# Performance work log

Hardware: AMD Instinct MI355X
Metric: run time of the kernel (lower is better)

## Reference

```python
import jax, jax.numpy as jnp
import numpy as np

# Dims: L list entries, T hutch samples, D = output_dim*inducing_size, H = 16 hidden
L, T, D, H = 32, 64, 8192, 16


def setup_inputs() -> dict:
    key = jax.random.key(0)
    k = jax.random.split(key, 4)
    return {
        "u": jax.random.normal(k[0], (L, D), jnp.float32),
        "w": jax.random.normal(k[1], (L, T, D), jnp.float32),  # Hutchinson Gaussian probes
        "W1": jax.random.normal(k[2], (H, D), jnp.float32) / np.sqrt(D).astype(np.float32),
        "b1": jnp.zeros((H,), jnp.float32),
        "W2": jax.random.normal(k[3], (D, H), jnp.float32) / np.sqrt(H).astype(np.float32),
        "b2": jnp.zeros((D,), jnp.float32),
    }


def reference(u, w, W1, b1, W2, b2):
    # f = W2 tanh(W1 u + b1) + b2 ; Jacobian J = W2 diag(1 - h^2) W1
    h = jnp.tanh(u @ W1.T + b1)                 # [L, H]
    f = h @ W2.T + b2                           # [L, D]  (f_u_list stacked)
    s = 1.0 - h * h                             # tanh' at preactivation, [L, H]
    # u_grad = J^T w  computed without materializing J: W1^T diag(s) W2^T w
    v = jnp.einsum('ltd,dh->lth', w, W2)        # W2^T w, [L, T, H]
    v = v * s[:, None, :]                       # diag(s) applied
    g = jnp.einsum('lth,hd->ltd', v, W1)        # J^T w, [L, T, D]
    traces = jnp.sum(g * w, axis=-1)            # w^T J w, [L, T]
    # mean over hutch samples, then mean over list entries -> [1, 1] like torch.mm output
    trace_final_mean = jnp.mean(traces).reshape(1, 1)
    return f, trace_final_mean
```

## Files before the change

kernel.cpp:

```cpp
#include <hip/hip_runtime.h>

typedef __attribute__((ext_vector_type(8))) short bf16x8;
typedef __attribute__((ext_vector_type(4))) float f32x4;

namespace {
constexpr int L = 32, T = 64, D = 8192, H = 16;
constexpr int M = L * T;
constexpr int KP = 64;
constexpr int CHUNK = D / KP;

constexpr size_t WS_WH  = 0;
constexpr size_t WS_WL  = WS_WH + 32 * 8192 / 2;
constexpr size_t WS_PRE = WS_WL + 32 * 8192 / 2;
constexpr size_t WS_AC  = WS_PRE + 32 * 8 * 16;
}

__device__ inline void split1(float f, short& h, short& l) {
  unsigned b = __float_as_uint(f);
  h = (short)(b >> 16);
  float lf = f - __uint_as_float(b & 0xFFFF0000u);
  l = (short)(__float_as_uint(lf) >> 16);
}

__device__ inline void split8(float4 a0, float4 a1, bf16x8& h, bf16x8& l) {
  float f[8] = {a0.x, a0.y, a0.z, a0.w, a1.x, a1.y, a1.z, a1.w};
#pragma unroll
  for (int i = 0; i < 8; ++i) {
    short hh, ll;
    split1(f[i], hh, ll);
    h[i] = hh; l[i] = ll;
  }
}

__global__ __launch_bounds__(256) void k_setup(
    const float* __restrict__ u, const float* __restrict__ W1,
    const float* __restrict__ W2,
    ushort* __restrict__ wh, ushort* __restrict__ wl,
    float* __restrict__ pre, float* __restrict__ out) {
  int b = blockIdx.x, tid = threadIdx.x;
  if (b == 0 && tid == 0) out[(size_t)L * D] = 0.f;
  if (b < 32) {
    int d = b * 256 + tid;
    const float4* src = reinterpret_cast<const float4*>(W2 + (size_t)d * 16);
    float4 q0 = src[0], q1 = src[1], q2 = src[2], q3 = src[3];
    float v[16] = {q0.x, q0.y, q0.z, q0.w, q1.x, q1.y, q1.z, q1.w,
                   q2.x, q2.y, q2.z, q2.w, q3.x, q3.y, q3.z, q3.w};
#pragma unroll
    for (int c = 0; c < 16; ++c) {
      short hh, ll;
      split1(v[c], hh, ll);
      wh[(size_t)c * D + d] = (ushort)hh;
      wl[(size_t)c * D + d] = (ushort)ll;
    }
  } else if (b < 64) {
    int q = (b - 32) * 256 + tid;
#pragma unroll
    for (int j = 0; j < 4; ++j) {
      int idx = (q + j * 8192) * 4;
      float4 qv = *reinterpret_cast<const float4*>(W1 + idx);
      short h0, l0, h1, l1, h2, l2, h3, l3;
      split1(qv.x, h0, l0); split1(qv.y, h1, l1);
      split1(qv.z, h2, l2); split1(qv.w, h3, l3);
      ushort4 vh = {(ushort)h0, (ushort)h1, (ushort)h2, (ushort)h3};
      ushort4 vl = {(ushort)l0, (ushort)l1, (ushort)l2, (ushort)l3};
      *reinterpret_cast<ushort4*>(wh + (size_t)16 * D + idx) = vh;
      *reinterpret_cast<ushort4*>(wl + (size_t)16 * D + idx) = vl;
    }
  } else {
    int bb = b - 64;
    int kc = bb & 7, l = bb >> 3;
    int d = kc * 1024 + tid * 4;
    float4 uv = *reinterpret_cast<const float4*>(u + (size_t)l * D + d);
    float acc[16];
#pragma unroll
    for (int h = 0; h < 16; ++h) {
      float4 wv = *reinterpret_cast<const float4*>(W1 + (size_t)h * D + d);
      float t = fmaf(uv.x, wv.x, 0.f);
      t = fmaf(uv.y, wv.y, t);
      t = fmaf(uv.z, wv.z, t);
      acc[h] = fmaf(uv.w, wv.w, t);
    }
#pragma unroll
    for (int h = 0; h < 16; ++h)
      for (int off = 1; off < 64; off <<= 1) acc[h] += __shfl_xor(acc[h], off);
    __shared__ float red[4][16];
    int lane = tid & 63, wv_ = tid >> 6;
    if (lane == 0) {
#pragma unroll
      for (int h = 0; h < 16; ++h) red[wv_][h] = acc[h];
    }
    __syncthreads();
    if (tid < 16)
      pre[((size_t)l * 8 + kc) * 16 + tid] =
          red[0][tid] + red[1][tid] + red[2][tid] + red[3][tid];
  }
}

__global__ __launch_bounds__(256) void k_trace_ac(
    const float* __restrict__ w,
    const ushort* __restrict__ wh, const ushort* __restrict__ wl,
    float* __restrict__ ac) {
  int tid = threadIdx.x;
  int wave = tid >> 6, lane = tid & 63;
  int lrow = lane & 15, kg = lane >> 4;
  int kp = blockIdx.x;
  int rt = blockIdx.y * 4 + wave;
  int m0 = rt * 16;
  int k0 = kp * CHUNK;

  const float*  wrow = w  + (size_t)(m0 + lrow) * D + k0 + kg * 8;
  const ushort* bh0  = wh + (size_t)lrow * D + k0 + kg * 8;
  const ushort* bl0  = wl + (size_t)lrow * D + k0 + kg * 8;
  const ushort* bh1  = bh0 + (size_t)16 * D;
  const ushort* bl1  = bl0 + (size_t)16 * D;

  f32x4 acc0 = {0.f, 0.f, 0.f, 0.f};
  f32x4 acc1 = {0.f, 0.f, 0.f, 0.f};

#pragma unroll
  for (int kk = 0; kk < CHUNK / 32; ++kk) {
    int off = kk * 32;
    float4 a0 = *reinterpret_cast<const float4*>(wrow + off);
    float4 a1 = *reinterpret_cast<const float4*>(wrow + off + 4);
    bf16x8 ah, al;
    split8(a0, a1, ah, al);
    bf16x8 vbh0 = *reinterpret_cast<const bf16x8*>(bh0 + off);
    bf16x8 vbl0 = *reinterpret_cast<const bf16x8*>(bl0 + off);
    bf16x8 vbh1 = *reinterpret_cast<const bf16x8*>(bh1 + off);
    bf16x8 vbl1 = *reinterpret_cast<const bf16x8*>(bl1 + off);
    acc0 = __builtin_amdgcn_mfma_f32_16x16x32_bf16(ah, vbh0, acc0, 0, 0, 0);
    acc0 = __builtin_amdgcn_mfma_f32_16x16x32_bf16(ah, vbl0, acc0, 0, 0, 0);
    acc0 = __builtin_amdgcn_mfma_f32_16x16x32_bf16(al, vbh0, acc0, 0, 0, 0);
    acc1 = __builtin_amdgcn_mfma_f32_16x16x32_bf16(ah, vbh1, acc1, 0, 0, 0);
    acc1 = __builtin_amdgcn_mfma_f32_16x16x32_bf16(ah, vbl1, acc1, 0, 0, 0);
    acc1 = __builtin_amdgcn_mfma_f32_16x16x32_bf16(al, vbh1, acc1, 0, 0, 0);
  }

  float* dst = ac + ((size_t)kp * M + m0 + kg * 4) * 32;
#pragma unroll
  for (int j = 0; j < 4; ++j) {
    dst[(size_t)j * 32 + lrow]      = acc0[j];
    dst[(size_t)j * 32 + 16 + lrow] = acc1[j];
  }
}

__global__ __launch_bounds__(256) void k_tail(
    const float* __restrict__ pre, const float* __restrict__ b1,
    const float* __restrict__ W2, const float* __restrict__ b2,
    const float* __restrict__ ac, float* __restrict__ out) {
  __shared__ float hl[8][16];
  __shared__ float s[16];
  __shared__ float red[4];
  int b = blockIdx.x, tid = threadIdx.x;
  if (b >= 128) {
    int bb = b - 128;
    int l = bb >> 3;
    if (tid < 16) {
      float p = b1[tid];
#pragma unroll
      for (int kc = 0; kc < 8; ++kc) p += pre[((size_t)l * 8 + kc) * 16 + tid];
      float t = tanhf(p);
      s[tid] = 1.f - t * t;
    }
    __syncthreads();
    int r = tid >> 5, c = tid & 31;
    size_t m = (size_t)bb * 8 + r;
    float acc = 0.f;
#pragma unroll 8
    for (int kp = 0; kp < KP; ++kp)
      acc += ac[((size_t)kp * M + m) * 32 + c];
    float partner = __shfl_xor(acc, 16);
    float t = (c < 16) ? s[c] * acc * partner : 0.f;
#pragma unroll
    for (int off = 1; off < 64; off <<= 1) t += __shfl_xor(t, off);
    int lane = tid & 63, wv_ = tid >> 6;
    if (lane == 0) red[wv_] = t;
    __syncthreads();
    if (tid == 0)
      atomicAdd(out + (size_t)L * D,
                (red[0] + red[1] + red[2] + red[3]) * (1.0f / (float)(L * T)));
    return;
  }
  int lg = b >> 5;
  if (tid < 128) {
    int ll = tid >> 4, h = tid & 15, l = lg * 8 + ll;
    float p = b1[h];
#pragma unroll
    for (int kc = 0; kc < 8; ++kc) p += pre[((size_t)l * 8 + kc) * 16 + h];
    hl[ll][h] = tanhf(p);
  }
  __syncthreads();
  int d = (b & 31) * 256 + tid;
  const float4* w2r = reinterpret_cast<const float4*>(W2 + (size_t)d * 16);
  float4 q0 = w2r[0], q1 = w2r[1], q2 = w2r[2], q3 = w2r[3];
  float w2v[16] = {q0.x, q0.y, q0.z, q0.w, q1.x, q1.y, q1.z, q1.w,
                   q2.x, q2.y, q2.z, q2.w, q3.x, q3.y, q3.z, q3.w};
  float bv = b2[d];
#pragma unroll
  for (int ll = 0; ll < 8; ++ll) {
    float fv = bv;
#pragma unroll
    for (int h = 0; h < 16; ++h) fv = fmaf(hl[ll][h], w2v[h], fv);
    out[(size_t)(lg * 8 + ll) * D + d] = fv;
  }
}

extern "C" void kernel_launch(void* const* d_in, const int* in_sizes, int n_in,
                              void* d_out, int out_size, void* d_ws, size_t ws_size,
                              hipStream_t stream) {
  const float* u  = (const float*)d_in[0];
  const float* w  = (const float*)d_in[1];
  const float* W1 = (const float*)d_in[2];
  const float* b1 = (const float*)d_in[3];
  const float* W2 = (const float*)d_in[4];
  const float* b2 = (const float*)d_in[5];
  float* out = (float*)d_out;
  float* ws  = (float*)d_ws;
  ushort* wcat_h = (ushort*)(ws + WS_WH);
  ushort* wcat_l = (ushort*)(ws + WS_WL);
  float* pre = ws + WS_PRE;
  float* acb = ws + WS_AC;

  hipLaunchKernelGGL(k_setup,    dim3(320), dim3(256), 0, stream,
                     u, W1, W2, wcat_h, wcat_l, pre, out);
  hipLaunchKernelGGL(k_trace_ac, dim3(KP, 32), dim3(256), 0, stream,
                     w, wcat_h, wcat_l, acb);
  hipLaunchKernelGGL(k_tail,     dim3(384), dim3(256), 0, stream,
                     pre, b1, W2, b2, acb, out);
}
```

Baseline: 132.6 us.

## Stage w and weight tiles through double-buffered swizzled LDS with atomic split-K reduction

Rewrites the main trace GEMM kernel. Each block now loads 32-row tiles of w and the split weight tiles into double-buffered, XOR-swizzled shared memory, converting fp32 to hi/lo bf16 once per element, and overlaps the next tile's global loads with MFMA compute. The K split drops from 64 to 4, and partial results are summed with atomicAdd into a buffer that the setup kernel zeroes, instead of writing 64 partial slabs that the tail kernel had to sum. The cost is LDS traffic and barriers, float atomics that make the summation order nondeterministic, and fewer blocks (256 instead of 2048), which lowers parallelism for a kernel bound by streaming the 64 MB w tensor.

Result: slower. 141.7 us (+6.9%).

```diff
diff --git a/kernel.cpp b/kernel.cpp
--- a/kernel.cpp
+++ b/kernel.cpp
@@ -6,8 +6,10 @@
 namespace {
 constexpr int L = 32, T = 64, D = 8192, H = 16;
 constexpr int M = L * T;
-constexpr int KP = 64;
-constexpr int CHUNK = D / KP;
+constexpr int KSPLIT = 4;
+constexpr int TK = 256;
+constexpr int NT = D / KSPLIT / TK;
+constexpr int BROWS = 32;
 
 constexpr size_t WS_WH  = 0;
 constexpr size_t WS_WL  = WS_WH + 32 * 8192 / 2;
@@ -22,21 +24,12 @@
   l = (short)(__float_as_uint(lf) >> 16);
 }
 
-__device__ inline void split8(float4 a0, float4 a1, bf16x8& h, bf16x8& l) {
-  float f[8] = {a0.x, a0.y, a0.z, a0.w, a1.x, a1.y, a1.z, a1.w};
-#pragma unroll
-  for (int i = 0; i < 8; ++i) {
-    short hh, ll;
-    split1(f[i], hh, ll);
-    h[i] = hh; l[i] = ll;
-  }
-}
-
 __global__ __launch_bounds__(256) void k_setup(
     const float* __restrict__ u, const float* __restrict__ W1,
     const float* __restrict__ W2,
     ushort* __restrict__ wh, ushort* __restrict__ wl,
-    float* __restrict__ pre, float* __restrict__ out) {
+    float* __restrict__ pre, float* __restrict__ ac,
+    float* __restrict__ out) {
   int b = blockIdx.x, tid = threadIdx.x;
   if (b == 0 && tid == 0) out[(size_t)L * D] = 0.f;
   if (b < 32) {
@@ -66,8 +59,14 @@
       *reinterpret_cast<ushort4*>(wh + (size_t)16 * D + idx) = vh;
       *reinterpret_cast<ushort4*>(wl + (size_t)16 * D + idx) = vl;
     }
+  } else if (b < 80) {
+    int t = (b - 64) * 256 + tid;
+    float4 z = {0.f, 0.f, 0.f, 0.f};
+    float4* dst = reinterpret_cast<float4*>(ac);
+#pragma unroll
+    for (int j = 0; j < 4; ++j) dst[t + j * 4096] = z;
   } else {
-    int bb = b - 64;
+    int bb = b - 80;
     int kc = bb & 7, l = bb >> 3;
     int d = kc * 1024 + tid * 4;
     float4 uv = *reinterpret_cast<const float4*>(u + (size_t)l * D + d);
@@ -96,51 +95,104 @@
   }
 }
 
-__global__ __launch_bounds__(256) void k_trace_ac(
+__global__ __launch_bounds__(256) void k_trace_lds(
     const float* __restrict__ w,
     const ushort* __restrict__ wh, const ushort* __restrict__ wl,
     float* __restrict__ ac) {
-  int tid = threadIdx.x;
-  int wave = tid >> 6, lane = tid & 63;
-  int lrow = lane & 15, kg = lane >> 4;
-  int kp = blockIdx.x;
-  int rt = blockIdx.y * 4 + wave;
-  int m0 = rt * 16;
-  int k0 = kp * CHUNK;
-
-  const float*  wrow = w  + (size_t)(m0 + lrow) * D + k0 + kg * 8;
-  const ushort* bh0  = wh + (size_t)lrow * D + k0 + kg * 8;
-  const ushort* bl0  = wl + (size_t)lrow * D + k0 + kg * 8;
-  const ushort* bh1  = bh0 + (size_t)16 * D;
-  const ushort* bl1  = bl0 + (size_t)16 * D;
+  __shared__ ushort sAh[2][BROWS][TK];
+  __shared__ ushort sAl[2][BROWS][TK];
+  __shared__ ushort sBh[2][32][TK];
+  __shared__ ushort sBl[2][32][TK];
+
+  const int tid = threadIdx.x;
+  const int wv = tid >> 6, lane = tid & 63;
+  const int lrow = lane & 15, kg = lane >> 4;
+  const int rt = wv & 1, kh = wv >> 1;
+  const int m0 = blockIdx.y * BROWS;
+  const int kbase = blockIdx.x * (NT * TK);
 
   f32x4 acc0 = {0.f, 0.f, 0.f, 0.f};
   f32x4 acc1 = {0.f, 0.f, 0.f, 0.f};
 
-#pragma unroll
-  for (int kk = 0; kk < CHUNK / 32; ++kk) {
-    int off = kk * 32;
-    float4 a0 = *reinterpret_cast<const float4*>(wrow + off);
-    float4 a1 = *reinterpret_cast<const float4*>(wrow + off + 4);
-    bf16x8 ah, al;
-    split8(a0, a1, ah, al);
-    bf16x8 vbh0 = *reinterpret_cast<const bf16x8*>(bh0 + off);
-    bf16x8 vbl0 = *reinterpret_cast<const bf16x8*>(bl0 + off);
-    bf16x8 vbh1 = *reinterpret_cast<const bf16x8*>(bh1 + off);
-    bf16x8 vbl1 = *reinterpret_cast<const bf16x8*>(bl1 + off);
-    acc0 = __builtin_amdgcn_mfma_f32_16x16x32_bf16(ah, vbh0, acc0, 0, 0, 0);
-    acc0 = __builtin_amdgcn_mfma_f32_16x16x32_bf16(ah, vbl0, acc0, 0, 0, 0);
-    acc0 = __builtin_amdgcn_mfma_f32_16x16x32_bf16(al, vbh0, acc0, 0, 0, 0);
-    acc1 = __builtin_amdgcn_mfma_f32_16x16x32_bf16(ah, vbh1, acc1, 0, 0, 0);
-    acc1 = __builtin_amdgcn_mfma_f32_16x16x32_bf16(ah, vbl1, acc1, 0, 0, 0);
-    acc1 = __builtin_amdgcn_mfma_f32_16x16x32_bf16(al, vbh1, acc1, 0, 0, 0);
-  }
-
-  float* dst = ac + ((size_t)kp * M + m0 + kg * 4) * 32;
+  float4 ar[8];
+  uint4  brh[4], brl[4];
+
+  auto stage_load = [&](int kt) {
+#pragma unroll
+    for (int j = 0; j < 8; ++j)
+      ar[j] = *reinterpret_cast<const float4*>(
+          w + (size_t)(m0 + j * 4 + wv) * D + kt + lane * 4);
+    int c0 = tid >> 5, ke = (tid & 31) * 8;
+#pragma unroll
+    for (int j = 0; j < 4; ++j) {
+      brh[j] = *reinterpret_cast<const uint4*>(wh + (size_t)(j * 8 + c0) * D + kt + ke);
+      brl[j] = *reinterpret_cast<const uint4*>(wl + (size_t)(j * 8 + c0) * D + kt + ke);
+    }
+  };
+  auto stage_write = [&](int buf) {
+#pragma unroll
+    for (int j = 0; j < 8; ++j) {
+      int row = j * 4 + wv;
+      int k = lane * 4;
+      int swk = k ^ ((row & 7) << 3);
+      short h0, l0, h1, l1, h2, l2, h3, l3;
+      split1(ar[j].x, h0, l0); split1(ar[j].y, h1, l1);
+      split1(ar[j].z, h2, l2); split1(ar[j].w, h3, l3);
+      ushort4 vh = {(ushort)h0, (ushort)h1, (ushort)h2, (ushort)h3};
+      ushort4 vl = {(ushort)l0, (ushort)l1, (ushort)l2, (ushort)l3};
+      *reinterpret_cast<ushort4*>(&sAh[buf][row][swk]) = vh;
+      *reinterpret_cast<ushort4*>(&sAl[buf][row][swk]) = vl;
+    }
+    int c0 = tid >> 5, ke = (tid & 31) * 8;
+#pragma unroll
+    for (int j = 0; j < 4; ++j) {
+      int row = j * 8 + c0;
+      int swk = ke ^ ((row & 7) << 3);
+      *reinterpret_cast<uint4*>(&sBh[buf][row][swk]) = brh[j];
+      *reinterpret_cast<uint4*>(&sBl[buf][row][swk]) = brl[j];
+    }
+  };
+  auto compute_tile = [&](int buf) {
+#pragma unroll
+    for (int kk = 0; kk < 4; ++kk) {
+      int k8 = kh * 128 + kk * 32 + kg * 8;
+      int rowA = rt * 16 + lrow;
+      int iA = k8 ^ ((rowA & 7) << 3);
+      int sB = (lrow & 7) << 3;
+      int iB = k8 ^ sB;
+      bf16x8 ah  = *reinterpret_cast<const bf16x8*>(&sAh[buf][rowA][iA]);
+      bf16x8 al  = *reinterpret_cast<const bf16x8*>(&sAl[buf][rowA][iA]);
+      bf16x8 bh0 = *reinterpret_cast<const bf16x8*>(&sBh[buf][lrow][iB]);
+      bf16x8 bl0 = *reinterpret_cast<const bf16x8*>(&sBl[buf][lrow][iB]);
+      bf16x8 bh1 = *reinterpret_cast<const bf16x8*>(&sBh[buf][16 + lrow][iB]);
+      bf16x8 bl1 = *reinterpret_cast<const bf16x8*>(&sBl[buf][16 + lrow][iB]);
+      acc0 = __builtin_amdgcn_mfma_f32_16x16x32_bf16(ah, bh0, acc0, 0, 0, 0);
+      acc1 = __builtin_amdgcn_mfma_f32_16x16x32_bf16(ah, bh1, acc1, 0, 0, 0);
+      acc0 = __builtin_amdgcn_mfma_f32_16x16x32_bf16(ah, bl0, acc0, 0, 0, 0);
+      acc1 = __builtin_amdgcn_mfma_f32_16x16x32_bf16(ah, bl1, acc1, 0, 0, 0);
+      acc0 = __builtin_amdgcn_mfma_f32_16x16x32_bf16(al, bh0, acc0, 0, 0, 0);
+      acc1 = __builtin_amdgcn_mfma_f32_16x16x32_bf16(al, bh1, acc1, 0, 0, 0);
+    }
+  };
+
+  stage_load(kbase);
+  stage_write(0);
+  __syncthreads();
+  int cur = 0;
+#pragma unroll
+  for (int t = 0; t < NT; ++t) {
+    if (t + 1 < NT) stage_load(kbase + (t + 1) * TK);
+    compute_tile(cur);
+    if (t + 1 < NT) stage_write(cur ^ 1);
+    __syncthreads();
+    cur ^= 1;
+  }
+
+  int mb = m0 + rt * 16 + kg * 4;
 #pragma unroll
   for (int j = 0; j < 4; ++j) {
-    dst[(size_t)j * 32 + lrow]      = acc0[j];
-    dst[(size_t)j * 32 + 16 + lrow] = acc1[j];
+    atomicAdd(ac + (size_t)(mb + j) * 32 + lrow,      acc0[j]);
+    atomicAdd(ac + (size_t)(mb + j) * 32 + 16 + lrow, acc1[j]);
   }
 }
 
@@ -164,11 +216,7 @@
     }
     __syncthreads();
     int r = tid >> 5, c = tid & 31;
-    size_t m = (size_t)bb * 8 + r;
-    float acc = 0.f;
-#pragma unroll 8
-    for (int kp = 0; kp < KP; ++kp)
-      acc += ac[((size_t)kp * M + m) * 32 + c];
+    float acc = ac[(size_t)bb * 256 + tid];
     float partner = __shfl_xor(acc, 16);
     float t = (c < 16) ? s[c] * acc * partner : 0.f;
 #pragma unroll
@@ -221,10 +269,10 @@
   float* pre = ws + WS_PRE;
   float* acb = ws + WS_AC;
 
-  hipLaunchKernelGGL(k_setup,    dim3(320), dim3(256), 0, stream,
-                     u, W1, W2, wcat_h, wcat_l, pre, out);
-  hipLaunchKernelGGL(k_trace_ac, dim3(KP, 32), dim3(256), 0, stream,
+  hipLaunchKernelGGL(k_setup,     dim3(336), dim3(256), 0, stream,
+                     u, W1, W2, wcat_h, wcat_l, pre, acb, out);
+  hipLaunchKernelGGL(k_trace_lds, dim3(KSPLIT, M / BROWS), dim3(256), 0, stream,
                      w, wcat_h, wcat_l, acb);
-  hipLaunchKernelGGL(k_tail,     dim3(384), dim3(256), 0, stream,
+  hipLaunchKernelGGL(k_tail,      dim3(384), dim3(256), 0, stream,
                      pre, b1, W2, b2, acb, out);
 }
```
